# Kernel tuning notes

Measured on AMD Instinct MI355X. Metric: run time of the kernel, lower is better.

The kernel has to match this reference:

```python
import jax, jax.numpy as jnp
import numpy as np

V, D, H, L, T_MAX = 95, 384, 6, 6, 256
HD = D // H  # 64
FF = 4 * D


def _layernorm(x, scale, bias, eps=1e-5):
    m = jnp.mean(x, axis=-1, keepdims=True)
    v = jnp.var(x, axis=-1, keepdims=True)
    return (x - m) * jax.lax.rsqrt(v + eps) * scale + bias


def setup_inputs() -> dict:
    key = jax.random.key(0)
    ks = iter(jax.random.split(key, 32))
    std = 0.02
    p = {
        "idx": jax.random.randint(next(ks), (128, 256), 0, V, dtype=jnp.int64)
               if jax.config.jax_enable_x64 else
               jax.random.randint(next(ks), (128, 256), 0, V, dtype=jnp.int32),
        "tok_emb": jax.random.normal(next(ks), (V, D), jnp.float32) * std,
        "pos_emb": jax.random.normal(next(ks), (T_MAX, D), jnp.float32) * std,
        # per-layer stacked params [L, ...]
        "ln1_s": jnp.ones((L, D), jnp.float32),
        "ln1_b": jnp.zeros((L, D), jnp.float32),
        "wq": jax.random.normal(next(ks), (L, D, D), jnp.float32) * std,
        "wk": jax.random.normal(next(ks), (L, D, D), jnp.float32) * std,
        "wv": jax.random.normal(next(ks), (L, D, D), jnp.float32) * std,
        "wo": jax.random.normal(next(ks), (L, D, D), jnp.float32) * std,
        "bo": jnp.zeros((L, D), jnp.float32),
        "ln2_s": jnp.ones((L, D), jnp.float32),
        "ln2_b": jnp.zeros((L, D), jnp.float32),
        "w1": jax.random.normal(next(ks), (L, D, FF), jnp.float32) * std,
        "b1": jnp.zeros((L, FF), jnp.float32),
        "w2": jax.random.normal(next(ks), (L, FF, D), jnp.float32) * std,
        "b2": jnp.zeros((L, D), jnp.float32),
        "lnf_s": jnp.ones((D,), jnp.float32),
        "lnf_b": jnp.zeros((D,), jnp.float32),
        "head_w": jax.random.normal(next(ks), (D, V), jnp.float32) * std,
        "head_b": jnp.zeros((V,), jnp.float32),
    }
    return p


def reference(idx, tok_emb, pos_emb, ln1_s, ln1_b, wq, wk, wv, wo, bo,
              ln2_s, ln2_b, w1, b1, w2, b2, lnf_s, lnf_b, head_w, head_b):
    B, T = idx.shape
    x = tok_emb[idx] + pos_emb[:T]  # [B,T,D]
    mask = jnp.tril(jnp.ones((T, T), bool))  # causal
    scale = HD ** -0.5

    def block(x, p):
        s1, b1n, Wq, Wk, Wv, Wo, Bo, s2, b2n, W1, B1, W2, B2 = p
        h = _layernorm(x, s1, b1n)
        q = (h @ Wq).reshape(B, T, H, HD)
        k = (h @ Wk).reshape(B, T, H, HD)
        v = (h @ Wv).reshape(B, T, H, HD)
        scores = jnp.einsum('bqhd,bkhd->bhqk', q, k) * scale
        scores = jnp.where(mask, scores, -jnp.inf)
        wei = jax.nn.softmax(scores, axis=-1)
        attn = jnp.einsum('bhqk,bkhd->bqhd', wei, v).reshape(B, T, D)
        x = x + attn @ Wo + Bo
        h2 = _layernorm(x, s2, b2n)
        x = x + jax.nn.relu(h2 @ W1 + B1) @ W2 + B2
        return x, None

    x, _ = jax.lax.scan(block, x, (ln1_s, ln1_b, wq, wk, wv, wo, bo,
                                   ln2_s, ln2_b, w1, b1, w2, b2))
    logits = _layernorm(x, lnf_s, lnf_b) @ head_w + head_b  # [B,T,V]
    return logits
```

## Files before the change

### kernel.cpp

```cpp
#include <hip/hip_runtime.h>
#include <hip/hip_bf16.h>
#include <cstdint>

#define DEV __device__ __forceinline__

typedef __hip_bfloat16 bf16;
typedef unsigned short u16;
typedef unsigned int u32;
typedef __attribute__((ext_vector_type(8))) short s8v;
typedef __attribute__((ext_vector_type(4))) float f4;

static constexpr int Bn = 128;
static constexpr int Tn = 256;
static constexpr int Dn = 384;
static constexpr int Hn = 6;
static constexpr int HDn = 64;
static constexpr int FFn = 1536;
static constexpr int Vn = 95;
static constexpr int Mn = Bn * 256;

DEV u16 f2b(float f) {
  bf16 h = __float2bfloat16(f);
  return *reinterpret_cast<u16*>(&h);
}
DEV u32 pk2(float a, float b) { return (u32)f2b(a) | ((u32)f2b(b) << 16); }

DEV void gl_lds16(const void* g, void* l) {
  auto gp = (const __attribute__((address_space(1))) u32*)(uintptr_t)g;
  auto lp = (__attribute__((address_space(3))) u32*)(u32)(uintptr_t)l;
  __builtin_amdgcn_global_load_lds(gp, lp, 16, 0, 0);
}

DEV void waitvm(int n) {
  if (n == 0)       asm volatile("s_waitcnt vmcnt(0)" ::: "memory");
  else if (n == 2)  asm volatile("s_waitcnt vmcnt(2)" ::: "memory");
  else if (n == 4)  asm volatile("s_waitcnt vmcnt(4)" ::: "memory");
  else if (n == 6)  asm volatile("s_waitcnt vmcnt(6)" ::: "memory");
  else if (n == 8)  asm volatile("s_waitcnt vmcnt(8)" ::: "memory");
  else if (n == 12) asm volatile("s_waitcnt vmcnt(12)" ::: "memory");
  else              asm volatile("s_waitcnt vmcnt(16)" ::: "memory");
}

template <int MODE, bool RELU, int NKT, int NT>
__global__ __launch_bounds__(256, 2) void gemm_h(
    const u16* __restrict__ A, const u16* __restrict__ Bw,
    const float* __restrict__ bias, const float* __restrict__ resid,
    void* __restrict__ outp)
{
  constexpr int K = NKT * 64;
  constexpr int N = NT * 16;
  constexpr int nTiles = NT / 8;
  __shared__ __align__(16) u16 As[3][128 * 64];
  const int tid = threadIdx.x;
  const int lane = tid & 63, wave = tid >> 6;
  const int quad = lane >> 4, l16 = lane & 15;
  const int wy = wave >> 1, wx = wave & 1;
  const int blk = blockIdx.x;
  const int xcd = blk & 7, tt = blk >> 3;
  const int nT = tt % nTiles, mT = xcd + 8 * (tt / nTiles);
  const int mBase = mT * 128, nBase = nT * 128;

  f4 acc[4][4] = {};

  int rS[4], cS[4];
#pragma unroll
  for (int i = 0; i < 4; i++) {
    int s = i * 256 + tid;
    rS[i] = s >> 3;
    cS[i] = ((s & 7) ^ (rS[i] & 7)) * 8;
  }

  const u16* Ab = A + (size_t)mBase * K;
  const u16* Bp = Bw + (size_t)((nBase >> 4) + wx * 4) * 512 + lane * 8;

#define STAGEA(buf, kt)                                                       \
  do {                                                                        \
    _Pragma("unroll")                                                         \
    for (int i = 0; i < 4; i++)                                               \
      gl_lds16(Ab + (size_t)rS[i] * K + (kt) + cS[i],                         \
               &As[buf][(i * 256 + wave * 64) * 8]);                          \
  } while (0)

  s8v bqa[2][4];
  STAGEA(0, 0);
  __builtin_amdgcn_sched_barrier(0);
#pragma unroll
  for (int j = 0; j < 4; j++)
    bqa[0][j] = *(const s8v*)(Bp + (size_t)0 * (NT * 512) + j * 512);
  __builtin_amdgcn_sched_barrier(0);
  STAGEA(1, 64);
  __builtin_amdgcn_sched_barrier(0);

  const int nk = NKT;
#pragma unroll
  for (int ik = 0; ik < nk; ik++) {
    const int cur = ik % 3;
    const int par = ik & 1;
    waitvm((ik + 1 < nk) ? 4 : 0);
    asm volatile("s_barrier" ::: "memory");
    s8v bqb[4];
#pragma unroll
    for (int j = 0; j < 4; j++)
      bqb[j] = *(const s8v*)(Bp + (size_t)(ik * 2 + 1) * (NT * 512) + j * 512);
    __builtin_amdgcn_sched_barrier(0);
    if (ik + 1 < nk) {
#pragma unroll
      for (int j = 0; j < 4; j++)
        bqa[par ^ 1][j] = *(const s8v*)(Bp + (size_t)(ik * 2 + 2) * (NT * 512) + j * 512);
    }
    __builtin_amdgcn_sched_barrier(0);
    if (ik + 2 < nk) STAGEA((ik + 2) % 3, (ik + 2) * 64);
    __builtin_amdgcn_sched_barrier(0);
    {
      s8v af[4];
#pragma unroll
      for (int i = 0; i < 4; i++) {
        int row = wy * 64 + i * 16 + l16;
        int ch = quad ^ (row & 7);
        af[i] = *(const s8v*)&As[cur][row * 64 + ch * 8];
      }
#pragma unroll
      for (int i = 0; i < 4; i++)
#pragma unroll
        for (int j = 0; j < 4; j++)
          acc[i][j] = __builtin_amdgcn_mfma_f32_16x16x32_bf16(af[i], bqa[par][j], acc[i][j], 0, 0, 0);
    }
    waitvm(4 * ((ik + 1 < nk) + (ik + 2 < nk)));
    {
      s8v af[4];
#pragma unroll
      for (int i = 0; i < 4; i++) {
        int row = wy * 64 + i * 16 + l16;
        int ch = (4 + quad) ^ (row & 7);
        af[i] = *(const s8v*)&As[cur][row * 64 + ch * 8];
      }
#pragma unroll
      for (int i = 0; i < 4; i++)
#pragma unroll
        for (int j = 0; j < 4; j++)
          acc[i][j] = __builtin_amdgcn_mfma_f32_16x16x32_bf16(af[i], bqb[j], acc[i][j], 0, 0, 0);
    }
  }
#undef STAGEA

  if (MODE == 0) {
    u16* out = (u16*)outp;
#pragma unroll
    for (int j = 0; j < 4; j++) {
      int n = nBase + wx * 64 + j * 16 + l16;
      float bv = bias ? bias[n] : 0.f;
#pragma unroll
      for (int i = 0; i < 4; i++) {
        int m0 = mBase + wy * 64 + i * 16 + quad * 4;
#pragma unroll
        for (int r = 0; r < 4; r++) {
          float v = acc[i][j][r] + bv;
          if (RELU) v = fmaxf(v, 0.f);
          out[(size_t)(m0 + r) * N + n] = f2b(v);
        }
      }
    }
  } else if (MODE == 3) {
    float* out = (float*)outp;
#pragma unroll
    for (int j = 0; j < 4; j++) {
      int n = nBase + wx * 64 + j * 16 + l16;
      if (n < Vn) {
        float bv = bias[n];
#pragma unroll
        for (int i = 0; i < 4; i++) {
          int m0 = mBase + wy * 64 + i * 16 + quad * 4;
#pragma unroll
          for (int r = 0; r < 4; r++)
            out[(size_t)(m0 + r) * Vn + n] = acc[i][j][r] + bv;
        }
      }
    }
  } else if (MODE == 4) {
    u16* qb = (u16*)outp;
    u16* kb = qb + (size_t)Mn * 384;
    u16* vb = kb + (size_t)Mn * 384;
#pragma unroll
    for (int j = 0; j < 4; j++) {
      int n = nBase + wx * 64 + j * 16 + l16;
      if (n < 768) {
        u16* dst = (n < 384) ? qb : kb;
        int col = (n < 384) ? n : (n - 384);
#pragma unroll
        for (int i = 0; i < 4; i++) {
          int m0 = mBase + wy * 64 + i * 16 + quad * 4;
#pragma unroll
          for (int r = 0; r < 4; r++)
            dst[(size_t)(m0 + r) * 384 + col] = f2b(acc[i][j][r]);
        }
      } else {
        int n7 = n - 768;
        int hh = n7 >> 6, d = n7 & 63;
#pragma unroll
        for (int i = 0; i < 4; i++) {
          int m0 = mBase + wy * 64 + i * 16 + quad * 4;
          int b = m0 >> 8, t0 = m0 & 255;
          uint2 w;
          w.x = pk2(acc[i][j][0], acc[i][j][1]);
          w.y = pk2(acc[i][j][2], acc[i][j][3]);
          *(uint2*)&vb[((b * Hn + hh) * HDn + d) * Tn + t0] = w;
        }
      }
    }
  }
}

template <int NKT>
__global__ __launch_bounds__(512, 2) void gemm_ln(
    const u16* __restrict__ A, const u16* __restrict__ Bw,
    const float* __restrict__ bias, const float* __restrict__ resid,
    float* __restrict__ xout,
    const float* __restrict__ sc, const float* __restrict__ bi,
    u16* __restrict__ hout)
{
  constexpr int K = NKT * 64;
  constexpr int NT = 24;
  __shared__ __align__(16) u16 As[2][128 * 64];
  __shared__ __align__(16) u16 Bs[2][24576];
  __shared__ float2 red[4][128];
  const int tid = threadIdx.x;
  const int lane = tid & 63, wave = tid >> 6;
  const int quad = lane >> 4, l16 = lane & 15;
  const int wy = wave >> 2, wx = wave & 3;
  const int blk = blockIdx.x;
  const int mT = (blk & 7) + 8 * (blk >> 3);
  const int mBase = mT * 128;

  f4 acc[4][6] = {};

  int rS[2], cS[2];
#pragma unroll
  for (int i = 0; i < 2; i++) {
    int s = i * 512 + tid;
    rS[i] = s >> 3;
    cS[i] = ((s & 7) ^ (rS[i] & 7)) * 8;
  }

  const u16* Ab = A + (size_t)mBase * K;

#define STAGEL(buf, kt)                                                       \
  do {                                                                        \
    _Pragma("unroll")                                                         \
    for (int i = 0; i < 2; i++)                                               \
      gl_lds16(Ab + (size_t)rS[i] * K + (kt) + cS[i],                         \
               &As[buf][(i * 512 + wave * 64) * 8]);                          \
  } while (0)

#define STAGEB2(buf, ikk)                                                     \
  do {                                                                        \
    _Pragma("unroll")                                                         \
    for (int L = 0; L < 6; L++) {                                             \
      int ks = L / 3, th = L % 3;                                             \
      int c = th * 4096 + tid * 8;                                            \
      gl_lds16(Bw + (size_t)((ikk) * 2 + ks) * (NT * 512) + c,                \
               &Bs[buf][ks * 12288 + c]);                                     \
    }                                                                         \
  } while (0)

  STAGEL(0, 0);
  STAGEB2(0, 0);

  const int nk = NKT;
#pragma unroll
  for (int ik = 0; ik < nk; ik++) {
    const int cur = ik & 1;
    asm volatile("s_waitcnt vmcnt(0)" ::: "memory");
    asm volatile("s_barrier" ::: "memory");
    if (ik + 1 < nk) {
      STAGEL(cur ^ 1, (ik + 1) * 64);
      STAGEB2(cur ^ 1, ik + 1);
    }
    __builtin_amdgcn_sched_barrier(0);
#pragma unroll
    for (int ks = 0; ks < 2; ks++) {
      s8v af[4], bq[6];
#pragma unroll
      for (int i = 0; i < 4; i++) {
        int row = wy * 64 + i * 16 + l16;
        int ch = (ks * 4 + quad) ^ (row & 7);
        af[i] = *(const s8v*)&As[cur][row * 64 + ch * 8];
      }
#pragma unroll
      for (int j = 0; j < 6; j++)
        bq[j] = *(const s8v*)&Bs[cur][ks * 12288 + (wx * 6 + j) * 512 + lane * 8];
#pragma unroll
      for (int i = 0; i < 4; i++)
#pragma unroll
        for (int j = 0; j < 6; j++)
          acc[i][j] = __builtin_amdgcn_mfma_f32_16x16x32_bf16(af[i], bq[j], acc[i][j], 0, 0, 0);
    }
  }
#undef STAGEL
#undef STAGEB2

  f4 psum[4] = {}, psq[4] = {};
#pragma unroll
  for (int j = 0; j < 6; j++) {
    int n = wx * 96 + j * 16 + l16;
    float bv = bias[n];
#pragma unroll
    for (int i = 0; i < 4; i++) {
      int m0 = mBase + wy * 64 + i * 16 + quad * 4;
#pragma unroll
      for (int r = 0; r < 4; r++) {
        int m = m0 + r;
        float v = resid[(size_t)m * Dn + n] + acc[i][j][r] + bv;
        xout[(size_t)m * Dn + n] = v;
        acc[i][j][r] = v;
        psum[i][r] += v;
        psq[i][r] += v * v;
      }
    }
  }
#pragma unroll
  for (int o = 1; o < 16; o <<= 1)
#pragma unroll
    for (int i = 0; i < 4; i++)
#pragma unroll
      for (int r = 0; r < 4; r++) {
        psum[i][r] += __shfl_xor(psum[i][r], o);
        psq[i][r] += __shfl_xor(psq[i][r], o);
      }
  if (l16 == 0) {
#pragma unroll
    for (int i = 0; i < 4; i++)
#pragma unroll
      for (int r = 0; r < 4; r++) {
        int lr = wy * 64 + i * 16 + quad * 4 + r;
        float2 p; p.x = psum[i][r]; p.y = psq[i][r];
        red[wx][lr] = p;
      }
  }
  __syncthreads();
  float scv[6], biv[6];
#pragma unroll
  for (int j = 0; j < 6; j++) {
    int n = wx * 96 + j * 16 + l16;
    scv[j] = sc[n];
    biv[j] = bi[n];
  }
#pragma unroll
  for (int i = 0; i < 4; i++)
#pragma unroll
    for (int r = 0; r < 4; r++) {
      int lr = wy * 64 + i * 16 + quad * 4 + r;
      float ts = 0.f, tq = 0.f;
#pragma unroll
      for (int w = 0; w < 4; w++) { float2 p = red[w][lr]; ts += p.x; tq += p.y; }
      float mean = ts * (1.f / 384.f);
      float inv = rsqrtf(tq * (1.f / 384.f) - mean * mean + 1e-5f);
      int m = mBase + lr;
#pragma unroll
      for (int j = 0; j < 6; j++) {
        int n = wx * 96 + j * 16 + l16;
        hout[(size_t)m * Dn + n] = f2b((acc[i][j][r] - mean) * inv * scv[j] + biv[j]);
      }
    }
}

__global__ __launch_bounds__(512, 2) void ffn_ln(
    const u16* __restrict__ A, const u16* __restrict__ B1w,
    const float* __restrict__ b1, const u16* __restrict__ B2w,
    const float* __restrict__ b2, const float* __restrict__ resid,
    float* __restrict__ xout,
    const float* __restrict__ sc, const float* __restrict__ bi,
    u16* __restrict__ hout)
{
  __shared__ __align__(16) u16 Hs[128 * 384];
  __shared__ __align__(16) u16 Ps[128 * 128];
  __shared__ float2 red[4][128];
  const int tid = threadIdx.x;
  const int lane = tid & 63, wave = tid >> 6;
  const int quad = lane >> 4, l16 = lane & 15;
  const int wy = wave >> 2, wx = wave & 3;
  const int mT = (blockIdx.x & 7) + 8 * (blockIdx.x >> 3);
  const int mBase = mT * 128;
  char* Psb = (char*)Ps;

  {
    const u16* hg = A + (size_t)mBase * Dn;
#pragma unroll
    for (int i = 0; i < 12; i++) {
      u32 S = i * 512 + tid;
      u32 row = S / 48u;
      u32 c = S - row * 48u;
      u32 srcc = (c & ~7u) | ((c & 7u) ^ (row & 7u));
      gl_lds16(hg + (size_t)row * Dn + srcc * 8, &Hs[S * 8]);
    }
  }
  asm volatile("s_waitcnt vmcnt(0)" ::: "memory");
  asm volatile("s_barrier" ::: "memory");

  f4 acc2[4][6] = {};
  const u16* B1p = B1w + (size_t)(wx * 2) * 512 + lane * 8;
  const u16* B2p = B2w + (size_t)(wx * 6) * 512 + lane * 8;
  s8v bq2[2][6];

#pragma unroll 1
  for (int c = 0; c < 12; c++) {
    float4 b1v0 = *(const float4*)&b1[c * 128 + wx * 32 + quad * 4];
    float4 b1v1 = *(const float4*)&b1[c * 128 + wx * 32 + 16 + quad * 4];
    __builtin_amdgcn_sched_barrier(0);
    s8v bq1[2][4];
#pragma unroll
    for (int u = 0; u < 4; u++) {
      int ks = u >> 1, j = u & 1;
      bq1[0][u] = *(const s8v*)(B1p + (size_t)(ks * 96 + c * 8 + j) * 512);
    }
    __builtin_amdgcn_sched_barrier(0);
    f4 acc1[4][2] = {};
#pragma unroll
    for (int ik = 0; ik < 6; ik++) {
      const int par = ik & 1;
      if (ik + 1 < 6) {
#pragma unroll
        for (int u = 0; u < 4; u++) {
          int ks = u >> 1, j = u & 1;
          bq1[par ^ 1][u] = *(const s8v*)(B1p + (size_t)(((ik + 1) * 2 + ks) * 96 + c * 8 + j) * 512);
        }
      }
      __builtin_amdgcn_sched_barrier(0);
      waitvm((ik + 1 < 6) ? 4 : 0);
#pragma unroll
      for (int ks = 0; ks < 2; ks++) {
        s8v af[4];
#pragma unroll
        for (int i = 0; i < 4; i++) {
          int row = wy * 64 + i * 16 + l16;
          int ch = ik * 8 + ((ks * 4 + quad) ^ (row & 7));
          af[i] = *(const s8v*)&Hs[row * 384 + ch * 8];
        }
#pragma unroll
        for (int i = 0; i < 4; i++)
#pragma unroll
          for (int j = 0; j < 2; j++)
            acc1[i][j] = __builtin_amdgcn_mfma_f32_16x16x32_bf16(
                bq1[par][ks * 2 + j], af[i], acc1[i][j], 0, 0, 0);
      }
    }
#pragma unroll
    for (int j = 0; j < 6; j++)
      bq2[0][j] = *(const s8v*)(B2p + (size_t)((c * 4) * 24 + j) * 512);
    __builtin_amdgcn_sched_barrier(0);
#pragma unroll
    for (int i = 0; i < 4; i++) {
      int m = wy * 64 + i * 16 + l16;
#pragma unroll
      for (int j = 0; j < 2; j++) {
        float4 bv4 = (j == 0) ? b1v0 : b1v1;
        float v0 = fmaxf(acc1[i][j][0] + bv4.x, 0.f);
        float v1 = fmaxf(acc1[i][j][1] + bv4.y, 0.f);
        float v2 = fmaxf(acc1[i][j][2] + bv4.z, 0.f);
        float v3 = fmaxf(acc1[i][j][3] + bv4.w, 0.f);
        uint2 w; w.x = pk2(v0, v1); w.y = pk2(v2, v3);
        int byteoff = (m * 256 + (wx * 32 + j * 16 + quad * 4) * 2) ^ ((m & 7) << 4);
        *(uint2*)(Psb + byteoff) = w;
      }
    }
    asm volatile("s_waitcnt lgkmcnt(0)" ::: "memory");
    asm volatile("s_barrier" ::: "memory");
#pragma unroll
    for (int ks2 = 0; ks2 < 4; ks2++) {
      const int p2 = ks2 & 1;
      if (ks2 + 1 < 4) {
#pragma unroll
        for (int j = 0; j < 6; j++)
          bq2[p2 ^ 1][j] = *(const s8v*)(B2p + (size_t)((c * 4 + ks2 + 1) * 24 + j) * 512);
      }
      __builtin_amdgcn_sched_barrier(0);
      waitvm((ks2 + 1 < 4) ? 6 : 0);
      s8v af2[4];
#pragma unroll
      for (int i = 0; i < 4; i++) {
        int m = wy * 64 + i * 16 + l16;
        int byteoff = (m * 256 + (ks2 * 4 + quad) * 16) ^ ((m & 7) << 4);
        af2[i] = *(const s8v*)(Psb + byteoff);
      }
#pragma unroll
      for (int i = 0; i < 4; i++)
#pragma unroll
        for (int j = 0; j < 6; j++)
          acc2[i][j] = __builtin_amdgcn_mfma_f32_16x16x32_bf16(
              af2[i], bq2[p2][j], acc2[i][j], 0, 0, 0);
    }
    asm volatile("s_waitcnt lgkmcnt(0)" ::: "memory");
    asm volatile("s_barrier" ::: "memory");
  }

  f4 psum[4] = {}, psq[4] = {};
#pragma unroll
  for (int j = 0; j < 6; j++) {
    int n = wx * 96 + j * 16 + l16;
    float bv = b2[n];
#pragma unroll
    for (int i = 0; i < 4; i++) {
      int m0 = mBase + wy * 64 + i * 16 + quad * 4;
#pragma unroll
      for (int r = 0; r < 4; r++) {
        int m = m0 + r;
        float v = resid[(size_t)m * Dn + n] + acc2[i][j][r] + bv;
        xout[(size_t)m * Dn + n] = v;
        acc2[i][j][r] = v;
        psum[i][r] += v;
        psq[i][r] += v * v;
      }
    }
  }
#pragma unroll
  for (int o = 1; o < 16; o <<= 1)
#pragma unroll
    for (int i = 0; i < 4; i++)
#pragma unroll
      for (int r = 0; r < 4; r++) {
        psum[i][r] += __shfl_xor(psum[i][r], o);
        psq[i][r] += __shfl_xor(psq[i][r], o);
      }
  if (l16 == 0) {
#pragma unroll
    for (int i = 0; i < 4; i++)
#pragma unroll
      for (int r = 0; r < 4; r++) {
        int lr = wy * 64 + i * 16 + quad * 4 + r;
        float2 p; p.x = psum[i][r]; p.y = psq[i][r];
        red[wx][lr] = p;
      }
  }
  __syncthreads();
  float scv[6], biv[6];
#pragma unroll
  for (int j = 0; j < 6; j++) {
    int n = wx * 96 + j * 16 + l16;
    scv[j] = sc[n];
    biv[j] = bi[n];
  }
#pragma unroll
  for (int i = 0; i < 4; i++)
#pragma unroll
    for (int r = 0; r < 4; r++) {
      int lr = wy * 64 + i * 16 + quad * 4 + r;
      float ts = 0.f, tq = 0.f;
#pragma unroll
      for (int w = 0; w < 4; w++) { float2 p = red[w][lr]; ts += p.x; tq += p.y; }
      float mean = ts * (1.f / 384.f);
      float inv = rsqrtf(tq * (1.f / 384.f) - mean * mean + 1e-5f);
      int m = mBase + lr;
#pragma unroll
      for (int j = 0; j < 6; j++) {
        int n = wx * 96 + j * 16 + l16;
        hout[(size_t)m * Dn + n] = f2b((acc2[i][j][r] - mean) * inv * scv[j] + biv[j]);
      }
    }
}

__global__ __launch_bounds__(256) void attn_kernel(
    const u16* __restrict__ q, const u16* __restrict__ k,
    const u16* __restrict__ vT, u16* __restrict__ ao)
{
  __shared__ __align__(16) u16 Psh[4][2][16 * 40];
  const int tid = threadIdx.x, lane = tid & 63, wave = tid >> 6;
  const int quad = lane >> 4, l16 = lane & 15;
  const int c4 = blockIdx.x / 768;
  const int bh = blockIdx.x - c4 * 768;
  const int b = bh / Hn, h = bh % Hn;
  const u16* qg = q + (b * Tn) * Dn + h * HDn;
  const u16* kg = k + (b * Tn) * Dn + h * HDn;
  const u16* vg = vT + bh * (HDn * Tn);
  u16* aog = ao + (b * Tn) * Dn + h * HDn;
  const float c1 = 0.125f * 1.44269504f;

  const int qt = (wave & 2) ? ((wave & 1) ? 15 - c4 : 8 + c4)
                            : ((wave & 1) ? 7 - c4 : c4);
  const int qglob = qt * 16 + l16;

  const s8v qf0 = *(const s8v*)&qg[qglob * Dn + quad * 8];
  const s8v qf1 = *(const s8v*)&qg[qglob * Dn + 32 + quad * 8];

  float lsum = 0.f;
  f4 O[4] = {};

  const int nch = qt / 2 + 1;
  for (int c2 = 0; c2 < nch; c2++) {
    const int kk0 = c2 * 32;
    f4 S0 = {0.f, 0.f, 0.f, 0.f}, S1 = S0;
    {
      s8v kf = *(const s8v*)&kg[(kk0 + l16) * Dn + quad * 8];
      S0 = __builtin_amdgcn_mfma_f32_16x16x32_bf16(kf, qf0, S0, 0, 0, 0);
      kf = *(const s8v*)&kg[(kk0 + l16) * Dn + 32 + quad * 8];
      S0 = __builtin_amdgcn_mfma_f32_16x16x32_bf16(kf, qf1, S0, 0, 0, 0);
    }
    if (kk0 + 16 <= qt * 16) {
      s8v kf = *(const s8v*)&kg[(kk0 + 16 + l16) * Dn + quad * 8];
      S1 = __builtin_amdgcn_mfma_f32_16x16x32_bf16(kf, qf0, S1, 0, 0, 0);
      kf = *(const s8v*)&kg[(kk0 + 16 + l16) * Dn + 32 + quad * 8];
      S1 = __builtin_amdgcn_mfma_f32_16x16x32_bf16(kf, qf1, S1, 0, 0, 0);
    }
    const int kkq = kk0 + quad * 4;
    f4 E0, E1;
#pragma unroll
    for (int r = 0; r < 4; r++) {
      E0[r] = (kkq + r <= qglob) ? exp2f(S0[r] * c1) : 0.f;
      E1[r] = (kkq + 16 + r <= qglob) ? exp2f(S1[r] * c1) : 0.f;
      lsum += E0[r] + E1[r];
    }
    u16* prow = &Psh[wave][c2 & 1][l16 * 40];
    uint2 w0, w1;
    w0.x = pk2(E0[0], E0[1]); w0.y = pk2(E0[2], E0[3]);
    w1.x = pk2(E1[0], E1[1]); w1.y = pk2(E1[2], E1[3]);
    *(uint2*)&prow[quad * 4] = w0;
    *(uint2*)&prow[16 + quad * 4] = w1;
    const s8v pf = *(const s8v*)&prow[quad * 8];
#pragma unroll
    for (int dm = 0; dm < 4; dm++) {
      s8v vf = *(const s8v*)&vg[(dm * 16 + l16) * Tn + kk0 + quad * 8];
      O[dm] = __builtin_amdgcn_mfma_f32_16x16x32_bf16(vf, pf, O[dm], 0, 0, 0);
    }
  }

  lsum += __shfl_xor(lsum, 16);
  lsum += __shfl_xor(lsum, 32);
  const float inv = 1.0f / lsum;
#pragma unroll
  for (int dm = 0; dm < 4; dm++) {
    uint2 w;
    w.x = pk2(O[dm][0] * inv, O[dm][1] * inv);
    w.y = pk2(O[dm][2] * inv, O[dm][3] * inv);
    *(uint2*)&aog[qglob * Dn + dm * 16 + quad * 4] = w;
  }
}

__global__ __launch_bounds__(256) void ln_kernel(
    const float* __restrict__ x, const float* __restrict__ sc,
    const float* __restrict__ bi, u16* __restrict__ out)
{
  int tok = blockIdx.x * 4 + (threadIdx.x >> 6);
  int lane = threadIdx.x & 63;
  const float* xr = x + (size_t)tok * Dn;
  float v[6];
  float s = 0.f, sq = 0.f;
#pragma unroll
  for (int i = 0; i < 6; i++) {
    v[i] = xr[lane + 64 * i];
    s += v[i];
    sq += v[i] * v[i];
  }
#pragma unroll
  for (int o = 1; o < 64; o <<= 1) {
    s += __shfl_xor(s, o);
    sq += __shfl_xor(sq, o);
  }
  float mean = s * (1.f / 384.f);
  float var = sq * (1.f / 384.f) - mean * mean;
  float inv = rsqrtf(var + 1e-5f);
  u16* orow = out + (size_t)tok * Dn;
#pragma unroll
  for (int i = 0; i < 6; i++) {
    int c = lane + 64 * i;
    orow[c] = f2b((v[i] - mean) * inv * sc[c] + bi[c]);
  }
}

__global__ __launch_bounds__(256) void embed_kernel(
    const int* __restrict__ idx, const float* __restrict__ tok,
    const float* __restrict__ pos, float* __restrict__ x)
{
  int i = blockIdx.x * 256 + threadIdx.x;
  int m = i / 96, c = (i - m * 96) * 4;
  int t = m & (Tn - 1);
  const float4 tv = *(const float4*)&tok[idx[m] * Dn + c];
  const float4 pv = *(const float4*)&pos[t * Dn + c];
  float4 r;
  r.x = tv.x + pv.x; r.y = tv.y + pv.y; r.z = tv.z + pv.z; r.w = tv.w + pv.w;
  *(float4*)&x[m * Dn + c] = r;
}

__global__ __launch_bounds__(256) void tcvt_frag(
    const float* __restrict__ src, u16* __restrict__ dst,
    int K, int C, int NTsub, int NTtot, int ntoff, int total)
{
  int t = blockIdx.x * 256 + threadIdx.x;
  if (t >= total) return;
  int j8 = t & 7;
  int lane = (t >> 3) & 63;
  int rest = t >> 9;
  int nt = rest % NTsub;
  int lkc = rest / NTsub;
  int KC = K >> 5;
  int kc = lkc % KC;
  int l = lkc / KC;
  int quad = lane >> 4, l16 = lane & 15;
  int k = kc * 32 + quad * 8 + j8;
  int n = nt * 16 + l16;
  float v = (n < C) ? src[((size_t)l * K + k) * C + n] : 0.f;
  dst[((size_t)(l * KC + kc) * NTtot + ntoff + nt) * 512 + lane * 8 + j8] = f2b(v);
}

extern "C" void kernel_launch(void* const* d_in, const int* in_sizes, int n_in,
                              void* d_out, int out_size, void* d_ws, size_t ws_size,
                              hipStream_t stream)
{
  (void)in_sizes; (void)n_in; (void)out_size;
  const int*   idx     = (const int*)d_in[0];
  const float* tok_emb = (const float*)d_in[1];
  const float* pos_emb = (const float*)d_in[2];
  const float* ln1_s   = (const float*)d_in[3];
  const float* ln1_b   = (const float*)d_in[4];
  const float* wq      = (const float*)d_in[5];
  const float* wk      = (const float*)d_in[6];
  const float* wv      = (const float*)d_in[7];
  const float* wo      = (const float*)d_in[8];
  const float* bo      = (const float*)d_in[9];
  const float* ln2_s   = (const float*)d_in[10];
  const float* ln2_b   = (const float*)d_in[11];
  const float* w1      = (const float*)d_in[12];
  const float* b1      = (const float*)d_in[13];
  const float* w2      = (const float*)d_in[14];
  const float* b2      = (const float*)d_in[15];
  const float* lnf_s   = (const float*)d_in[16];
  const float* lnf_b   = (const float*)d_in[17];
  const float* head_w  = (const float*)d_in[18];
  const float* head_b  = (const float*)d_in[19];
  float* out = (float*)d_out;

  char* ws = (char*)d_ws;
  float* x  = (float*)(ws + 0);
  u16*   h  = (u16*)(ws + 50331648);
  u16*   qb = (u16*)(ws + 75497472);
  u16*   kb = (u16*)(ws + 100663296);
  u16*   vb = (u16*)(ws + 125829120);
  u16*   ab = (u16*)(ws + 150994944);
  u16* qkvT = (u16*)(ws + 176160768);
  u16* woT  = qkvT + 6 * 442368;
  u16* w1T  = woT + 6 * 147456;
  u16* w2T  = w1T + 6 * 589824;
  u16* hdT  = w2T + 6 * 589824;
  if (ws_size < (size_t)197492736) return;

  int tot = 6 * 384 * 384;
  tcvt_frag<<<(tot + 255) / 256, 256, 0, stream>>>(wq, qkvT, 384, 384, 24, 72, 0, tot);
  tcvt_frag<<<(tot + 255) / 256, 256, 0, stream>>>(wk, qkvT, 384, 384, 24, 72, 24, tot);
  tcvt_frag<<<(tot + 255) / 256, 256, 0, stream>>>(wv, qkvT, 384, 384, 24, 72, 48, tot);
  tcvt_frag<<<(tot + 255) / 256, 256, 0, stream>>>(wo, woT, 384, 384, 24, 24, 0, tot);
  tot = 6 * 384 * 1536;
  tcvt_frag<<<(tot + 255) / 256, 256, 0, stream>>>(w1, w1T, 384, 1536, 96, 96, 0, tot);
  tcvt_frag<<<(tot + 255) / 256, 256, 0, stream>>>(w2, w2T, 1536, 384, 24, 24, 0, tot);
  tot = 384 * 128;
  tcvt_frag<<<(tot + 255) / 256, 256, 0, stream>>>(head_w, hdT, 384, 95, 8, 8, 0, tot);

  embed_kernel<<<(Mn * 96) / 256, 256, 0, stream>>>(idx, tok_emb, pos_emb, x);
  ln_kernel<<<Mn / 4, 256, 0, stream>>>(x, ln1_s, ln1_b, h);

  for (int l = 0; l < 6; l++) {
    gemm_h<4, false, 6, 72><<<2304, 256, 0, stream>>>(h, qkvT + l * 442368, nullptr, nullptr, qb);
    attn_kernel<<<Bn * Hn * 4, 256, 0, stream>>>(qb, kb, vb, ab);
    gemm_ln<6><<<256, 512, 0, stream>>>(ab, woT + l * 147456, bo + l * Dn, x, x,
                                        ln2_s + l * Dn, ln2_b + l * Dn, h);
    const float* ns = (l < 5) ? (ln1_s + (l + 1) * Dn) : lnf_s;
    const float* nb = (l < 5) ? (ln1_b + (l + 1) * Dn) : lnf_b;
    ffn_ln<<<256, 512, 0, stream>>>(h, w1T + l * 589824, b1 + l * FFn,
                                    w2T + l * 589824, b2 + l * Dn,
                                    x, x, ns, nb, h);
  }
  gemm_h<3, false, 6, 8><<<256, 256, 0, stream>>>(h, hdT, head_b, nullptr, out);
}
```

Before: 1.458 ms.

## Halve ffn_ln row tile to 64 rows and double grid for occupancy

The fused FFN+LayerNorm kernel now processes 64-row tiles with all 8 waves split across columns instead of 128 rows split 2x4, and launches 512 blocks instead of 256. Each wave handles fewer output columns, so it needs fewer accumulators and B-fragment buffers. LDS per block is roughly halved, and launch bounds request 4 blocks per CU to raise occupancy and fill more CUs. The cost is that each weight fragment is reused over half as many rows, which doubles total weight traffic from global memory/L2.

```diff
diff --git a/kernel.cpp b/kernel.cpp
--- a/kernel.cpp
+++ b/kernel.cpp
@@ -34,6 +34,7 @@
 DEV void waitvm(int n) {
   if (n == 0)       asm volatile("s_waitcnt vmcnt(0)" ::: "memory");
   else if (n == 2)  asm volatile("s_waitcnt vmcnt(2)" ::: "memory");
+  else if (n == 3)  asm volatile("s_waitcnt vmcnt(3)" ::: "memory");
   else if (n == 4)  asm volatile("s_waitcnt vmcnt(4)" ::: "memory");
   else if (n == 6)  asm volatile("s_waitcnt vmcnt(6)" ::: "memory");
   else if (n == 8)  asm volatile("s_waitcnt vmcnt(8)" ::: "memory");
@@ -363,7 +364,7 @@
     }
 }
 
-__global__ __launch_bounds__(512, 2) void ffn_ln(
+__global__ __launch_bounds__(512, 4) void ffn_ln(
     const u16* __restrict__ A, const u16* __restrict__ B1w,
     const float* __restrict__ b1, const u16* __restrict__ B2w,
     const float* __restrict__ b2, const float* __restrict__ resid,
@@ -371,21 +372,21 @@
     const float* __restrict__ sc, const float* __restrict__ bi,
     u16* __restrict__ hout)
 {
-  __shared__ __align__(16) u16 Hs[128 * 384];
-  __shared__ __align__(16) u16 Ps[128 * 128];
-  __shared__ float2 red[4][128];
+  __shared__ __align__(16) u16 Hs[64 * 384];
+  __shared__ __align__(16) u16 Ps[64 * 128];
+  __shared__ float2 red[8][64];
   const int tid = threadIdx.x;
   const int lane = tid & 63, wave = tid >> 6;
   const int quad = lane >> 4, l16 = lane & 15;
-  const int wy = wave >> 2, wx = wave & 3;
+  const int wx = wave;
   const int mT = (blockIdx.x & 7) + 8 * (blockIdx.x >> 3);
-  const int mBase = mT * 128;
+  const int mBase = mT * 64;
   char* Psb = (char*)Ps;
 
   {
     const u16* hg = A + (size_t)mBase * Dn;
 #pragma unroll
-    for (int i = 0; i < 12; i++) {
+    for (int i = 0; i < 6; i++) {
       u32 S = i * 512 + tid;
       u32 row = S / 48u;
       u32 c = S - row * 48u;
@@ -396,71 +397,60 @@
   asm volatile("s_waitcnt vmcnt(0)" ::: "memory");
   asm volatile("s_barrier" ::: "memory");
 
-  f4 acc2[4][6] = {};
-  const u16* B1p = B1w + (size_t)(wx * 2) * 512 + lane * 8;
-  const u16* B2p = B2w + (size_t)(wx * 6) * 512 + lane * 8;
-  s8v bq2[2][6];
+  f4 acc2[4][3] = {};
+  const u16* B1p = B1w + lane * 8;
+  const u16* B2p = B2w + lane * 8;
+  s8v bq2[2][3];
 
 #pragma unroll 1
   for (int c = 0; c < 12; c++) {
-    float4 b1v0 = *(const float4*)&b1[c * 128 + wx * 32 + quad * 4];
-    float4 b1v1 = *(const float4*)&b1[c * 128 + wx * 32 + 16 + quad * 4];
+    float4 b1v = *(const float4*)&b1[c * 128 + wx * 16 + quad * 4];
     __builtin_amdgcn_sched_barrier(0);
-    s8v bq1[2][4];
-#pragma unroll
-    for (int u = 0; u < 4; u++) {
-      int ks = u >> 1, j = u & 1;
-      bq1[0][u] = *(const s8v*)(B1p + (size_t)(ks * 96 + c * 8 + j) * 512);
-    }
+    s8v bq1[2][2];
+#pragma unroll
+    for (int ks = 0; ks < 2; ks++)
+      bq1[0][ks] = *(const s8v*)(B1p + (size_t)(ks * 96 + c * 8 + wx) * 512);
     __builtin_amdgcn_sched_barrier(0);
-    f4 acc1[4][2] = {};
+    f4 acc1[4] = {};
 #pragma unroll
     for (int ik = 0; ik < 6; ik++) {
       const int par = ik & 1;
       if (ik + 1 < 6) {
 #pragma unroll
-        for (int u = 0; u < 4; u++) {
-          int ks = u >> 1, j = u & 1;
-          bq1[par ^ 1][u] = *(const s8v*)(B1p + (size_t)(((ik + 1) * 2 + ks) * 96 + c * 8 + j) * 512);
-        }
+        for (int ks = 0; ks < 2; ks++)
+          bq1[par ^ 1][ks] = *(const s8v*)(B1p + (size_t)(((ik + 1) * 2 + ks) * 96 + c * 8 + wx) * 512);
       }
       __builtin_amdgcn_sched_barrier(0);
-      waitvm((ik + 1 < 6) ? 4 : 0);
+      waitvm((ik + 1 < 6) ? 2 : 0);
 #pragma unroll
       for (int ks = 0; ks < 2; ks++) {
         s8v af[4];
 #pragma unroll
         for (int i = 0; i < 4; i++) {
-          int row = wy * 64 + i * 16 + l16;
+          int row = i * 16 + l16;
           int ch = ik * 8 + ((ks * 4 + quad) ^ (row & 7));
           af[i] = *(const s8v*)&Hs[row * 384 + ch * 8];
         }
 #pragma unroll
         for (int i = 0; i < 4; i++)
-#pragma unroll
-          for (int j = 0; j < 2; j++)
-            acc1[i][j] = __builtin_amdgcn_mfma_f32_16x16x32_bf16(
-                bq1[par][ks * 2 + j], af[i], acc1[i][j], 0, 0, 0);
-      }
-    }
-#pragma unroll
-    for (int j = 0; j < 6; j++)
-      bq2[0][j] = *(const s8v*)(B2p + (size_t)((c * 4) * 24 + j) * 512);
+          acc1[i] = __builtin_amdgcn_mfma_f32_16x16x32_bf16(
+              bq1[par][ks], af[i], acc1[i], 0, 0, 0);
+      }
+    }
+#pragma unroll
+    for (int j = 0; j < 3; j++)
+      bq2[0][j] = *(const s8v*)(B2p + (size_t)((c * 4) * 24 + wx * 3 + j) * 512);
     __builtin_amdgcn_sched_barrier(0);
 #pragma unroll
     for (int i = 0; i < 4; i++) {
-      int m = wy * 64 + i * 16 + l16;
-#pragma unroll
-      for (int j = 0; j < 2; j++) {
-        float4 bv4 = (j == 0) ? b1v0 : b1v1;
-        float v0 = fmaxf(acc1[i][j][0] + bv4.x, 0.f);
-        float v1 = fmaxf(acc1[i][j][1] + bv4.y, 0.f);
-        float v2 = fmaxf(acc1[i][j][2] + bv4.z, 0.f);
-        float v3 = fmaxf(acc1[i][j][3] + bv4.w, 0.f);
-        uint2 w; w.x = pk2(v0, v1); w.y = pk2(v2, v3);
-        int byteoff = (m * 256 + (wx * 32 + j * 16 + quad * 4) * 2) ^ ((m & 7) << 4);
-        *(uint2*)(Psb + byteoff) = w;
-      }
+      int m = i * 16 + l16;
+      float v0 = fmaxf(acc1[i][0] + b1v.x, 0.f);
+      float v1 = fmaxf(acc1[i][1] + b1v.y, 0.f);
+      float v2 = fmaxf(acc1[i][2] + b1v.z, 0.f);
+      float v3 = fmaxf(acc1[i][3] + b1v.w, 0.f);
+      uint2 w; w.x = pk2(v0, v1); w.y = pk2(v2, v3);
+      int byteoff = (m * 256 + (wx * 16 + quad * 4) * 2) ^ ((m & 7) << 4);
+      *(uint2*)(Psb + byteoff) = w;
     }
     asm volatile("s_waitcnt lgkmcnt(0)" ::: "memory");
     asm volatile("s_barrier" ::: "memory");
@@ -469,22 +459,22 @@
       const int p2 = ks2 & 1;
       if (ks2 + 1 < 4) {
 #pragma unroll
-        for (int j = 0; j < 6; j++)
-          bq2[p2 ^ 1][j] = *(const s8v*)(B2p + (size_t)((c * 4 + ks2 + 1) * 24 + j) * 512);
+        for (int j = 0; j < 3; j++)
+          bq2[p2 ^ 1][j] = *(const s8v*)(B2p + (size_t)((c * 4 + ks2 + 1) * 24 + wx * 3 + j) * 512);
       }
       __builtin_amdgcn_sched_barrier(0);
-      waitvm((ks2 + 1 < 4) ? 6 : 0);
+      waitvm((ks2 + 1 < 4) ? 3 : 0);
       s8v af2[4];
 #pragma unroll
       for (int i = 0; i < 4; i++) {
-        int m = wy * 64 + i * 16 + l16;
+        int m = i * 16 + l16;
         int byteoff = (m * 256 + (ks2 * 4 + quad) * 16) ^ ((m & 7) << 4);
         af2[i] = *(const s8v*)(Psb + byteoff);
       }
 #pragma unroll
       for (int i = 0; i < 4; i++)
 #pragma unroll
-        for (int j = 0; j < 6; j++)
+        for (int j = 0; j < 3; j++)
           acc2[i][j] = __builtin_amdgcn_mfma_f32_16x16x32_bf16(
               af2[i], bq2[p2][j], acc2[i][j], 0, 0, 0);
     }
@@ -494,12 +484,12 @@
 
   f4 psum[4] = {}, psq[4] = {};
 #pragma unroll
-  for (int j = 0; j < 6; j++) {
-    int n = wx * 96 + j * 16 + l16;
+  for (int j = 0; j < 3; j++) {
+    int n = wx * 48 + j * 16 + l16;
     float bv = b2[n];
 #pragma unroll
     for (int i = 0; i < 4; i++) {
-      int m0 = mBase + wy * 64 + i * 16 + quad * 4;
+      int m0 = mBase + i * 16 + quad * 4;
 #pragma unroll
       for (int r = 0; r < 4; r++) {
         int m = m0 + r;
@@ -525,16 +515,16 @@
     for (int i = 0; i < 4; i++)
 #pragma unroll
       for (int r = 0; r < 4; r++) {
-        int lr = wy * 64 + i * 16 + quad * 4 + r;
+        int lr = i * 16 + quad * 4 + r;
         float2 p; p.x = psum[i][r]; p.y = psq[i][r];
         red[wx][lr] = p;
       }
   }
   __syncthreads();
-  float scv[6], biv[6];
-#pragma unroll
-  for (int j = 0; j < 6; j++) {
-    int n = wx * 96 + j * 16 + l16;
+  float scv[3], biv[3];
+#pragma unroll
+  for (int j = 0; j < 3; j++) {
+    int n = wx * 48 + j * 16 + l16;
     scv[j] = sc[n];
     biv[j] = bi[n];
   }
@@ -542,16 +532,16 @@
   for (int i = 0; i < 4; i++)
 #pragma unroll
     for (int r = 0; r < 4; r++) {
-      int lr = wy * 64 + i * 16 + quad * 4 + r;
+      int lr = i * 16 + quad * 4 + r;
       float ts = 0.f, tq = 0.f;
 #pragma unroll
-      for (int w = 0; w < 4; w++) { float2 p = red[w][lr]; ts += p.x; tq += p.y; }
+      for (int w = 0; w < 8; w++) { float2 p = red[w][lr]; ts += p.x; tq += p.y; }
       float mean = ts * (1.f / 384.f);
       float inv = rsqrtf(tq * (1.f / 384.f) - mean * mean + 1e-5f);
       int m = mBase + lr;
 #pragma unroll
-      for (int j = 0; j < 6; j++) {
-        int n = wx * 96 + j * 16 + l16;
+      for (int j = 0; j < 3; j++) {
+        int n = wx * 48 + j * 16 + l16;
         hout[(size_t)m * Dn + n] = f2b((acc2[i][j][r] - mean) * inv * scv[j] + biv[j]);
       }
     }
@@ -761,7 +751,7 @@
                                         ln2_s + l * Dn, ln2_b + l * Dn, h);
     const float* ns = (l < 5) ? (ln1_s + (l + 1) * Dn) : lnf_s;
     const float* nb = (l < 5) ? (ln1_b + (l + 1) * Dn) : lnf_b;
-    ffn_ln<<<256, 512, 0, stream>>>(h, w1T + l * 589824, b1 + l * FFn,
+    ffn_ln<<<512, 512, 0, stream>>>(h, w1T + l * 589824, b1 + l * FFn,
                                     w2T + l * 589824, b2 + l * Dn,
                                     x, x, ns, nb, h);
   }
```

Result: slower. 1.612 ms (+10.6%).

## Software-pipeline FFN chunks with double-buffered P tile and direct global A loads

Applied to the files above, without the earlier changes.

Drops the LDS staging of the 128x384 LN output tile in the fused FFN kernel and reads A fragments straight from global memory. The freed shared memory holds a double-buffered hidden-activation tile, so the second GEMM for chunk c-1 runs in the same segment as the first GEMM for chunk c, leaving one barrier per segment instead of two. It also removes the manual register double-buffering, sched_barriers and explicit vmcnt waits on weight loads and leaves load scheduling to the compiler. This trades LDS capacity and a barrier for repeated global or L2 reads of A, which are now done once per FF chunk and may be poorly coalesced.

```diff
diff --git a/kernel.cpp b/kernel.cpp
--- a/kernel.cpp
+++ b/kernel.cpp
@@ -371,8 +371,7 @@
     const float* __restrict__ sc, const float* __restrict__ bi,
     u16* __restrict__ hout)
 {
-  __shared__ __align__(16) u16 Hs[128 * 384];
-  __shared__ __align__(16) u16 Ps[128 * 128];
+  __shared__ __align__(16) u16 Ps[2][128 * 128];
   __shared__ float2 red[4][128];
   const int tid = threadIdx.x;
   const int lane = tid & 63, wave = tid >> 6;
@@ -380,113 +379,80 @@
   const int wy = wave >> 2, wx = wave & 3;
   const int mT = (blockIdx.x & 7) + 8 * (blockIdx.x >> 3);
   const int mBase = mT * 128;
-  char* Psb = (char*)Ps;
-
-  {
-    const u16* hg = A + (size_t)mBase * Dn;
-#pragma unroll
-    for (int i = 0; i < 12; i++) {
-      u32 S = i * 512 + tid;
-      u32 row = S / 48u;
-      u32 c = S - row * 48u;
-      u32 srcc = (c & ~7u) | ((c & 7u) ^ (row & 7u));
-      gl_lds16(hg + (size_t)row * Dn + srcc * 8, &Hs[S * 8]);
-    }
-  }
-  asm volatile("s_waitcnt vmcnt(0)" ::: "memory");
-  asm volatile("s_barrier" ::: "memory");
-
-  f4 acc2[4][6] = {};
+
+  const u16* hg = A + (size_t)mBase * Dn;
   const u16* B1p = B1w + (size_t)(wx * 2) * 512 + lane * 8;
   const u16* B2p = B2w + (size_t)(wx * 6) * 512 + lane * 8;
-  s8v bq2[2][6];
+
+  f4 acc2[4][6] = {};
 
 #pragma unroll 1
-  for (int c = 0; c < 12; c++) {
-    float4 b1v0 = *(const float4*)&b1[c * 128 + wx * 32 + quad * 4];
-    float4 b1v1 = *(const float4*)&b1[c * 128 + wx * 32 + 16 + quad * 4];
-    __builtin_amdgcn_sched_barrier(0);
-    s8v bq1[2][4];
-#pragma unroll
-    for (int u = 0; u < 4; u++) {
-      int ks = u >> 1, j = u & 1;
-      bq1[0][u] = *(const s8v*)(B1p + (size_t)(ks * 96 + c * 8 + j) * 512);
-    }
-    __builtin_amdgcn_sched_barrier(0);
-    f4 acc1[4][2] = {};
-#pragma unroll
-    for (int ik = 0; ik < 6; ik++) {
-      const int par = ik & 1;
-      if (ik + 1 < 6) {
-#pragma unroll
-        for (int u = 0; u < 4; u++) {
-          int ks = u >> 1, j = u & 1;
-          bq1[par ^ 1][u] = *(const s8v*)(B1p + (size_t)(((ik + 1) * 2 + ks) * 96 + c * 8 + j) * 512);
+  for (int seg = 0; seg <= 12; seg++) {
+    if (seg < 12) {
+      const int c = seg;
+      float4 b1v0 = *(const float4*)&b1[c * 128 + wx * 32 + quad * 4];
+      float4 b1v1 = *(const float4*)&b1[c * 128 + wx * 32 + 16 + quad * 4];
+      f4 acc1[4][2] = {};
+#pragma unroll
+      for (int ik = 0; ik < 6; ik++) {
+#pragma unroll
+        for (int ks = 0; ks < 2; ks++) {
+          s8v bq1[2], af[4];
+#pragma unroll
+          for (int j = 0; j < 2; j++)
+            bq1[j] = *(const s8v*)(B1p + (size_t)((ik * 2 + ks) * 96 + c * 8 + j) * 512);
+#pragma unroll
+          for (int i = 0; i < 4; i++) {
+            int row = wy * 64 + i * 16 + l16;
+            af[i] = *(const s8v*)&hg[(size_t)row * Dn + ik * 64 + ks * 32 + quad * 8];
+          }
+#pragma unroll
+          for (int i = 0; i < 4; i++)
+#pragma unroll
+            for (int j = 0; j < 2; j++)
+              acc1[i][j] = __builtin_amdgcn_mfma_f32_16x16x32_bf16(
+                  bq1[j], af[i], acc1[i][j], 0, 0, 0);
         }
       }
-      __builtin_amdgcn_sched_barrier(0);
-      waitvm((ik + 1 < 6) ? 4 : 0);
-#pragma unroll
-      for (int ks = 0; ks < 2; ks++) {
-        s8v af[4];
-#pragma unroll
-        for (int i = 0; i < 4; i++) {
-          int row = wy * 64 + i * 16 + l16;
-          int ch = ik * 8 + ((ks * 4 + quad) ^ (row & 7));
-          af[i] = *(const s8v*)&Hs[row * 384 + ch * 8];
-        }
-#pragma unroll
-        for (int i = 0; i < 4; i++)
-#pragma unroll
-          for (int j = 0; j < 2; j++)
-            acc1[i][j] = __builtin_amdgcn_mfma_f32_16x16x32_bf16(
-                bq1[par][ks * 2 + j], af[i], acc1[i][j], 0, 0, 0);
-      }
-    }
-#pragma unroll
-    for (int j = 0; j < 6; j++)
-      bq2[0][j] = *(const s8v*)(B2p + (size_t)((c * 4) * 24 + j) * 512);
-    __builtin_amdgcn_sched_barrier(0);
-#pragma unroll
-    for (int i = 0; i < 4; i++) {
-      int m = wy * 64 + i * 16 + l16;
-#pragma unroll
-      for (int j = 0; j < 2; j++) {
-        float4 bv4 = (j == 0) ? b1v0 : b1v1;
-        float v0 = fmaxf(acc1[i][j][0] + bv4.x, 0.f);
-        float v1 = fmaxf(acc1[i][j][1] + bv4.y, 0.f);
-        float v2 = fmaxf(acc1[i][j][2] + bv4.z, 0.f);
-        float v3 = fmaxf(acc1[i][j][3] + bv4.w, 0.f);
-        uint2 w; w.x = pk2(v0, v1); w.y = pk2(v2, v3);
-        int byteoff = (m * 256 + (wx * 32 + j * 16 + quad * 4) * 2) ^ ((m & 7) << 4);
-        *(uint2*)(Psb + byteoff) = w;
-      }
-    }
-    asm volatile("s_waitcnt lgkmcnt(0)" ::: "memory");
-    asm volatile("s_barrier" ::: "memory");
-#pragma unroll
-    for (int ks2 = 0; ks2 < 4; ks2++) {
-      const int p2 = ks2 & 1;
-      if (ks2 + 1 < 4) {
-#pragma unroll
-        for (int j = 0; j < 6; j++)
-          bq2[p2 ^ 1][j] = *(const s8v*)(B2p + (size_t)((c * 4 + ks2 + 1) * 24 + j) * 512);
-      }
-      __builtin_amdgcn_sched_barrier(0);
-      waitvm((ks2 + 1 < 4) ? 6 : 0);
-      s8v af2[4];
+      char* Pb = (char*)&Ps[c & 1][0];
 #pragma unroll
       for (int i = 0; i < 4; i++) {
         int m = wy * 64 + i * 16 + l16;
-        int byteoff = (m * 256 + (ks2 * 4 + quad) * 16) ^ ((m & 7) << 4);
-        af2[i] = *(const s8v*)(Psb + byteoff);
-      }
-#pragma unroll
-      for (int i = 0; i < 4; i++)
+#pragma unroll
+        for (int j = 0; j < 2; j++) {
+          float4 bv4 = (j == 0) ? b1v0 : b1v1;
+          float v0 = fmaxf(acc1[i][j][0] + bv4.x, 0.f);
+          float v1 = fmaxf(acc1[i][j][1] + bv4.y, 0.f);
+          float v2 = fmaxf(acc1[i][j][2] + bv4.z, 0.f);
+          float v3 = fmaxf(acc1[i][j][3] + bv4.w, 0.f);
+          uint2 w; w.x = pk2(v0, v1); w.y = pk2(v2, v3);
+          int byteoff = (m * 256 + (wx * 32 + j * 16 + quad * 4) * 2) ^ ((m & 7) << 4);
+          *(uint2*)(Pb + byteoff) = w;
+        }
+      }
+    }
+    if (seg >= 1) {
+      const int cc = seg - 1;
+      const char* Pb = (const char*)&Ps[cc & 1][0];
+#pragma unroll
+      for (int ks2 = 0; ks2 < 4; ks2++) {
+        s8v bq2[6], af2[4];
 #pragma unroll
         for (int j = 0; j < 6; j++)
-          acc2[i][j] = __builtin_amdgcn_mfma_f32_16x16x32_bf16(
-              af2[i], bq2[p2][j], acc2[i][j], 0, 0, 0);
+          bq2[j] = *(const s8v*)(B2p + (size_t)((cc * 4 + ks2) * 24 + j) * 512);
+#pragma unroll
+        for (int i = 0; i < 4; i++) {
+          int m = wy * 64 + i * 16 + l16;
+          int byteoff = (m * 256 + (ks2 * 4 + quad) * 16) ^ ((m & 7) << 4);
+          af2[i] = *(const s8v*)(Pb + byteoff);
+        }
+#pragma unroll
+        for (int i = 0; i < 4; i++)
+#pragma unroll
+          for (int j = 0; j < 6; j++)
+            acc2[i][j] = __builtin_amdgcn_mfma_f32_16x16x32_bf16(
+                af2[i], bq2[j], acc2[i][j], 0, 0, 0);
+      }
     }
     asm volatile("s_waitcnt lgkmcnt(0)" ::: "memory");
     asm volatile("s_barrier" ::: "memory");
```

Result: slower. 2.199 ms (+50.9%).
